# Performance work log

Hardware: AMD Instinct MI355X
Metric: run time of the kernel (lower is better)

## Reference

```python
import jax, jax.numpy as jnp
import numpy as np

N, E = 20000, 320000
D, DW, DS, NCLS = 512, 300, 16, 13


def setup_inputs() -> dict:
    key = jax.random.key(0)
    ks = jax.random.split(key, 24)
    g = lambda k, s, sc=0.02: (jax.random.normal(k, s, dtype=jnp.float32) * sc)
    inp = {
        'n_f': jax.random.normal(ks[0], (N, D), dtype=jnp.float32),
        'word2vec': jax.random.normal(ks[1], (N, DW), dtype=jnp.float32),
        's_f': jax.random.normal(ks[2], (E, DS), dtype=jnp.float32),
        'src': jax.random.randint(ks[3], (E,), 0, N, dtype=jnp.int32),
        'dst': jax.random.randint(ks[4], (E,), 0, N, dtype=jnp.int32),
        # edge MLPs: G_E_L_S=[2*D+DS, D], G_E_L_S2=[2*DW, D]
        'W_e': g(ks[5], (2 * D + DS, D)), 'b_e': jnp.zeros((D,), jnp.float32),
        'W_el': g(ks[6], (2 * DW, D)), 'b_el': jnp.zeros((D,), jnp.float32),
        # attention MLPs: G_A_L_S=[D,1], G_A_L_S2=[D,1]
        'W_a': g(ks[7], (D, 1)), 'b_a': jnp.zeros((1,), jnp.float32),
        'W_al': g(ks[8], (D, 1)), 'b_al': jnp.zeros((1,), jnp.float32),
        # node MLPs: G_N_L_S=[2*D, D], G_N_L_S2=[2*DW, DW]
        'W_n': g(ks[9], (2 * D, D)), 'b_n': jnp.zeros((D,), jnp.float32),
        'W_nl': g(ks[10], (2 * DW, DW)), 'b_nl': jnp.zeros((DW,), jnp.float32),
        # edge readout: G_ER_L_S=[2*D+2*DW+DS, D, 13], acts ['ReLU','Identity']
        'W_r1': g(ks[11], (2 * D + 2 * DW + DS, D)), 'b_r1': jnp.zeros((D,), jnp.float32),
        'W_r2': g(ks[12], (D, NCLS)), 'b_r2': jnp.zeros((NCLS,), jnp.float32),
    }
    return inp


def _segment_softmax(logits, seg, num_segments):
    m = jax.ops.segment_max(logits, seg, num_segments=num_segments)
    m = jnp.where(jnp.isfinite(m), m, 0.0)
    e = jnp.exp(logits - m[seg])
    s = jax.ops.segment_sum(e, seg, num_segments=num_segments)
    return e / (s[seg] + 1e-9)


def _forward(n_f, word2vec, s_f, W_e, b_e, W_el, b_el, W_a, b_a, W_al, b_al,
             W_n, b_n, W_nl, b_nl, W_r1, b_r1, W_r2, b_r2, src, dst):
    n = n_f.shape[0]
    relu = jax.nn.relu
    # H_H_EdgeApplyModule: e_f = ReLU(MLP([src n_f, s_f, dst n_f]))
    feat = jnp.concatenate([n_f[src], s_f, n_f[dst]], axis=1)            # [E, 2D+DS]
    e_f = relu(feat @ W_e + b_e)                                         # [E, D]
    feat_lang = jnp.concatenate([word2vec[src], word2vec[dst]], axis=1)  # [E, 2DW]
    e_f_lang = relu(feat_lang @ W_el + b_el)                             # [E, D]
    # E_AttentionModule1: LeakyReLU(0.2) attention logits per edge
    a = jax.nn.leaky_relu(e_f @ W_a + b_a, 0.2)[:, 0]
    a_l = jax.nn.leaky_relu(e_f_lang @ W_al + b_al, 0.2)[:, 0]
    # edge-softmax over incoming edges of each destination node
    alpha = _segment_softmax(a, dst, n)
    alpha_l = _segment_softmax(a_l, dst, n)
    # attention-weighted aggregation (scatter-add per dst node)
    z = jax.ops.segment_sum(alpha[:, None] * e_f, dst, num_segments=n)            # [N, D]
    z_l = jax.ops.segment_sum(alpha_l[:, None] * word2vec[src], dst, num_segments=n)  # [N, DW]
    # H_NodeApplyModule: node update with ReLU MLPs
    n_new = relu(jnp.concatenate([n_f, z], axis=1) @ W_n + b_n)          # [N, D]
    w_new = relu(jnp.concatenate([word2vec, z_l], axis=1) @ W_nl + b_nl) # [N, DW]
    # edge readout (G_ER): [src n_f, src w2v, s_f, dst w2v, dst n_f] -> ReLU -> Identity
    r = jnp.concatenate([n_new[src], w_new[src], s_f, w_new[dst], n_new[dst]], axis=1)
    h = relu(r @ W_r1 + b_r1)
    return h @ W_r2 + b_r2                                               # [E, 13]


def reference(n_f, word2vec, s_f, src, dst, W_e, b_e, W_el, b_el, W_a, b_a,
              W_al, b_al, W_n, b_n, W_nl, b_nl, W_r1, b_r1, W_r2, b_r2):
    return _forward(n_f, word2vec, s_f, W_e, b_e, W_el, b_el, W_a, b_a, W_al, b_al,
                    W_n, b_n, W_nl, b_nl, W_r1, b_r1, W_r2, b_r2, src, dst)
```

## Files before the change

kernel.cpp:

```cpp
#include <hip/hip_runtime.h>

typedef unsigned short u16;
typedef unsigned int u32;
typedef __bf16 bf16x8 __attribute__((ext_vector_type(8)));
typedef float f32x4 __attribute__((ext_vector_type(4)));

#define ND 512
#define DWR 300
#define DWP 320
#define NCLS 13

__device__ __forceinline__ float bf2f(u16 u) { return __uint_as_float(((u32)u) << 16); }
__device__ __forceinline__ u16 f2bf(float f) {
    u32 u = __float_as_uint(f);
    u32 r = (u + 0x7FFFu + ((u >> 16) & 1u)) >> 16;
    return (u16)r;
}
__device__ __forceinline__ void ub8(float4 r, float* v) {
    union { float4 f; u16 u[8]; } U; U.f = r;
#pragma unroll
    for (int k = 0; k < 8; ++k) v[k] = bf2f(U.u[k]);
}
__device__ __forceinline__ void ld8f(const u16* p, float* v) { ub8(*(const float4*)p, v); }
__device__ __forceinline__ void ld16(const float* p, float* s) {
    const float4* sp = (const float4*)p;
    float4 s0 = sp[0], s1 = sp[1], s2 = sp[2], s3 = sp[3];
    s[0]=s0.x; s[1]=s0.y; s[2]=s0.z; s[3]=s0.w; s[4]=s1.x; s[5]=s1.y; s[6]=s1.z; s[7]=s1.w;
    s[8]=s2.x; s[9]=s2.y; s[10]=s2.z; s[11]=s2.w; s[12]=s3.x; s[13]=s3.y; s[14]=s3.z; s[15]=s3.w;
}

struct GSeg { const u16* base; const int* idx; int stride; int width; };
struct GSegs { GSeg s[5]; };
struct TSeg { int src_begin; int wreal; int wpad; };
struct TSegs { TSeg t[5]; };

template<int RELU>
__global__ __launch_bounds__(256) void gemm_k(
    int M, int Nout, GSegs segs,
    const u16* __restrict__ BT, int ldb,
    const float* __restrict__ bias, int bias_n,
    u16* __restrict__ outb, int ldo)
{
    __shared__ __align__(16) u16 As[128 * 40];
    __shared__ __align__(16) u16 Bs[128 * 40];
    const int tid = threadIdx.x;

    const int gx = gridDim.x, gy = gridDim.y;
    const int g0 = blockIdx.x + gx * blockIdx.y;
    int xt, yt;
    {
        const int fullg = gx >> 3;
        const int gsz = 8 * gy;
        if (g0 < fullg * gsz) {
            const int grp = g0 / gsz, w = g0 % gsz;
            xt = grp * 8 + (w & 7); yt = w >> 3;
        } else {
            const int remx = gx - fullg * 8;
            const int t = g0 - fullg * gsz;
            xt = fullg * 8 + t % remx; yt = t / remx;
        }
    }
    const int m0 = xt * 128, n0 = yt * 128;

    const int row = tid >> 1, half = tid & 1;
    int mrow = m0 + row; if (mrow >= M) mrow = M - 1;
    const int lane = tid & 63, wid = tid >> 6;
    const int wr = (wid >> 1) * 64, wc = (wid & 1) * 64;
    const int lr = lane & 15, lg = lane >> 4;

    f32x4 acc[4][4];
    for (int fm = 0; fm < 4; fm++)
        for (int fn = 0; fn < 4; fn++)
            acc[fm][fn] = f32x4{0.f, 0.f, 0.f, 0.f};

    const u16* brow = BT + (size_t)(n0 + row) * ldb + half * 16;

    auto do_step = [&](const u16* ga_, const u16* gb_) {
        float4 a0 = *(const float4*)ga_;
        float4 a1 = *(const float4*)(ga_ + 8);
        float4 b0 = *(const float4*)gb_;
        float4 b1 = *(const float4*)(gb_ + 8);
        __syncthreads();
        *(float4*)&As[row * 40 + half * 16]     = a0;
        *(float4*)&As[row * 40 + half * 16 + 8] = a1;
        *(float4*)&Bs[row * 40 + half * 16]     = b0;
        *(float4*)&Bs[row * 40 + half * 16 + 8] = b1;
        __syncthreads();
        bf16x8 af[4], bfv[4];
#pragma unroll
        for (int f = 0; f < 4; f++) {
            af[f]  = *(const bf16x8*)&As[(wr + f * 16 + lr) * 40 + lg * 8];
            bfv[f] = *(const bf16x8*)&Bs[(wc + f * 16 + lr) * 40 + lg * 8];
        }
#pragma unroll
        for (int fm = 0; fm < 4; fm++)
#pragma unroll
            for (int fn = 0; fn < 4; fn++)
                acc[fm][fn] = __builtin_amdgcn_mfma_f32_16x16x32_bf16(af[fm], bfv[fn], acc[fm][fn], 0, 0, 0);
    };

    int k0 = 0;
#pragma unroll
    for (int sI = 0; sI < 5; sI++) {
        const GSeg S = segs.s[sI];
        if (S.width > 0) {
            const int ridx = S.idx ? S.idx[mrow] : mrow;
            const u16* abase = S.base + (size_t)ridx * S.stride + half * 16;
            for (int kk = 0; kk < S.width; kk += 32) {
                do_step(abase + kk, brow + k0 + kk);
            }
            k0 += S.width;
        }
    }

#pragma unroll
    for (int fm = 0; fm < 4; fm++) {
#pragma unroll
        for (int i = 0; i < 4; i++) {
            const int grow = m0 + wr + fm * 16 + lg * 4 + i;
            const bool rok = grow < M;
#pragma unroll
            for (int fn = 0; fn < 4; fn++) {
                const int col = n0 + wc + fn * 16 + lr;
                float v = acc[fm][fn][i];
                v += (col < bias_n) ? bias[col] : 0.f;
                if (RELU) v = fmaxf(v, 0.f);
                if (rok && col < Nout) outb[(size_t)grow * ldo + col] = f2bf(v);
            }
        }
    }
}

__global__ __launch_bounds__(256) void pass1_k(
    const u16* __restrict__ Q, const u16* __restrict__ Lq,
    const float* __restrict__ s_f, const float* __restrict__ wmid,
    const int* __restrict__ psrc, const int* __restrict__ pdst, const int* __restrict__ perm,
    const float* __restrict__ W_a, const float* __restrict__ W_al,
    const float* __restrict__ b_e, const float* __restrict__ b_el,
    const float* __restrict__ b_a, const float* __restrict__ b_al,
    float* __restrict__ aA, float* __restrict__ aL, int E)
{
    __shared__ __align__(16) u16 wmids[16 * 520];
    __shared__ __align__(16) u16 As_v[128 * 40];
    __shared__ __align__(16) u16 As_l[128 * 40];
    __shared__ float sfs[16 * 128];
    __shared__ float bes[512], bels[512];
    __shared__ __align__(16) u16 was[512], wals[512];

    const int tid = threadIdx.x;
    const int e0 = blockIdx.x * 128;

    for (int i = tid; i < 16 * 512; i += 256)
        wmids[(i >> 9) * 520 + (i & 511)] = f2bf(wmid[i]);
    for (int i = tid; i < 512; i += 256) {
        bes[i] = b_e[i]; bels[i] = b_el[i];
        was[i] = f2bf(W_a[i]); wals[i] = f2bf(W_al[i]);
    }

    const int row = tid >> 1, half = tid & 1;
    const int er = e0 + row;
    const int erc = (er < E) ? er : E - 1;
    {
        const int pe = perm[erc];
        const int jh = half * 8;
        const float4* sp = (const float4*)(s_f + (size_t)pe * 16 + jh);
        float4 a = sp[0], b = sp[1];
        sfs[(jh + 0) * 128 + row] = a.x; sfs[(jh + 1) * 128 + row] = a.y;
        sfs[(jh + 2) * 128 + row] = a.z; sfs[(jh + 3) * 128 + row] = a.w;
        sfs[(jh + 4) * 128 + row] = b.x; sfs[(jh + 5) * 128 + row] = b.y;
        sfs[(jh + 6) * 128 + row] = b.z; sfs[(jh + 7) * 128 + row] = b.w;
    }

    const int ps = psrc[erc], pd = pdst[erc];
    const u16* q1b = Q + (size_t)ps * 1024;
    const u16* q2b = Q + (size_t)pd * 1024 + 512;
    const u16* l1b = Lq + (size_t)ps * 1024;
    const u16* l2b = Lq + (size_t)pd * 1024 + 512;

    const int lane = tid & 63, wid = tid >> 6;
    const int lr = lane & 15, lg = lane >> 4;
    f32x4 accv[2], accl[2];
    accv[0] = accv[1] = accl[0] = accl[1] = f32x4{0.f, 0.f, 0.f, 0.f};

    union { bf16x8 v; float4 f; } BZ; BZ.f = float4{0.f, 0.f, 0.f, 0.f};

    __syncthreads();

    for (int ch = 0; ch < 16; ++ch) {
        const int k0 = ch * 32 + half * 16;
        float4 rq1a = *(const float4*)(q1b + k0);
        float4 rq1b = *(const float4*)(q1b + k0 + 8);
        float4 rq2a = *(const float4*)(q2b + k0);
        float4 rq2b = *(const float4*)(q2b + k0 + 8);
        float4 rl1a = *(const float4*)(l1b + k0);
        float4 rl1b = *(const float4*)(l1b + k0 + 8);
        float4 rl2a = *(const float4*)(l2b + k0);
        float4 rl2b = *(const float4*)(l2b + k0 + 8);

        float uv[16], ul[16], t1[8], t2[8];
        ub8(rq1a, t1); ub8(rq2a, t2);
#pragma unroll
        for (int k = 0; k < 8; ++k) uv[k] = t1[k] + t2[k] + bes[k0 + k];
        ub8(rq1b, t1); ub8(rq2b, t2);
#pragma unroll
        for (int k = 0; k < 8; ++k) uv[8 + k] = t1[k] + t2[k] + bes[k0 + 8 + k];
        ub8(rl1a, t1); ub8(rl2a, t2);
#pragma unroll
        for (int k = 0; k < 8; ++k) ul[k] = t1[k] + t2[k] + bels[k0 + k];
        ub8(rl1b, t1); ub8(rl2b, t2);
#pragma unroll
        for (int k = 0; k < 8; ++k) ul[8 + k] = t1[k] + t2[k] + bels[k0 + 8 + k];

#pragma unroll
        for (int j = 0; j < 16; ++j) {
            const float sv = sfs[j * 128 + row];
            union { float4 f; u16 u[8]; } W1, W2;
            W1.f = *(const float4*)&wmids[j * 520 + k0];
            W2.f = *(const float4*)&wmids[j * 520 + k0 + 8];
#pragma unroll
            for (int k = 0; k < 8; ++k) {
                uv[k]     = fmaf(sv, bf2f(W1.u[k]), uv[k]);
                uv[8 + k] = fmaf(sv, bf2f(W2.u[k]), uv[8 + k]);
            }
        }
        union { float4 f; u16 u[8]; } Va, Vb, La, Lb;
#pragma unroll
        for (int k = 0; k < 8; ++k) {
            Va.u[k] = f2bf(fmaxf(uv[k], 0.f));
            Vb.u[k] = f2bf(fmaxf(uv[8 + k], 0.f));
            La.u[k] = f2bf(fmaxf(ul[k], 0.f));
            Lb.u[k] = f2bf(fmaxf(ul[8 + k], 0.f));
        }
        __syncthreads();
        *(float4*)&As_v[row * 40 + half * 16]     = Va.f;
        *(float4*)&As_v[row * 40 + half * 16 + 8] = Vb.f;
        *(float4*)&As_l[row * 40 + half * 16]     = La.f;
        *(float4*)&As_l[row * 40 + half * 16 + 8] = Lb.f;
        __syncthreads();

        bf16x8 bv = BZ.v, bl = BZ.v;
        if (lr == 0) {
            bv = *(const bf16x8*)&was[ch * 32 + lg * 8];
            bl = *(const bf16x8*)&wals[ch * 32 + lg * 8];
        }
#pragma unroll
        for (int m = 0; m < 2; ++m) {
            bf16x8 afv = *(const bf16x8*)&As_v[(wid * 32 + m * 16 + lr) * 40 + lg * 8];
            bf16x8 afl = *(const bf16x8*)&As_l[(wid * 32 + m * 16 + lr) * 40 + lg * 8];
            accv[m] = __builtin_amdgcn_mfma_f32_16x16x32_bf16(afv, bv, accv[m], 0, 0, 0);
            accl[m] = __builtin_amdgcn_mfma_f32_16x16x32_bf16(afl, bl, accl[m], 0, 0, 0);
        }
    }

    if (lr == 0) {
        const float ba = b_a[0], bal = b_al[0];
#pragma unroll
        for (int m = 0; m < 2; ++m) {
#pragma unroll
            for (int i = 0; i < 4; ++i) {
                const int e = e0 + wid * 32 + m * 16 + lg * 4 + i;
                if (e < E) {
                    float x = accv[m][i] + ba;
                    aA[e] = x > 0.f ? x : 0.2f * x;
                    float y = accl[m][i] + bal;
                    aL[e] = y > 0.f ? y : 0.2f * y;
                }
            }
        }
    }
}

__global__ __launch_bounds__(256) void softmax_k(
    float* __restrict__ a, float* __restrict__ al,
    const int* __restrict__ offs, int N, int E)
{
    const int node = blockIdx.x * 4 + (threadIdx.x >> 6);
    if (node >= N) return;
    const int lane = threadIdx.x & 63;
    const int e0 = offs[node];
    const int e1 = (node + 1 < N) ? offs[node + 1] : E;
    if (e0 >= e1) return;
    float m = -3.4e38f, ml = -3.4e38f;
    for (int e = e0 + lane; e < e1; e += 64) { m = fmaxf(m, a[e]); ml = fmaxf(ml, al[e]); }
#pragma unroll
    for (int off = 32; off >= 1; off >>= 1) {
        m  = fmaxf(m,  __shfl_xor(m,  off, 64));
        ml = fmaxf(ml, __shfl_xor(ml, off, 64));
    }
    float s = 0.f, sl = 0.f;
    for (int e = e0 + lane; e < e1; e += 64) {
        float v = expf(a[e] - m);   a[e] = v;  s += v;
        float w = expf(al[e] - ml); al[e] = w; sl += w;
    }
#pragma unroll
    for (int off = 32; off >= 1; off >>= 1) {
        s  += __shfl_xor(s,  off, 64);
        sl += __shfl_xor(sl, off, 64);
    }
    const float rs = 1.f / (s + 1e-9f), rsl = 1.f / (sl + 1e-9f);
    for (int e = e0 + lane; e < e1; e += 64) { a[e] *= rs; al[e] *= rsl; }
}

__global__ __launch_bounds__(256) void passz_k(
    const u16* __restrict__ Q, const u16* __restrict__ wv_bf,
    const float* __restrict__ s_f, const float* __restrict__ wmid,
    const int* __restrict__ psrc, const int* __restrict__ perm, const int* __restrict__ offs,
    const float* __restrict__ alpha, const float* __restrict__ alphal,
    const float* __restrict__ b_e,
    u16* __restrict__ z_bf, u16* __restrict__ zl_bf, int N, int E)
{
    __shared__ __align__(16) u16 wmids[16 * 512];
    const int tid = threadIdx.x;
    for (int i = tid; i < 16 * 512; i += 256) wmids[i] = f2bf(wmid[i]);
    __syncthreads();
    const int node = blockIdx.x * 4 + (tid >> 6);
    if (node >= N) return;
    const int lane = tid & 63;
    const int col0 = lane * 8;
    const int colw = (lane < 40) ? col0 : 0;
    const int e0 = offs[node];
    const int e1 = (node + 1 < N) ? offs[node + 1] : E;

    float q2b[8], accz[8], accl[8], t[8];
    ld8f(Q + (size_t)node * 1024 + 512 + col0, q2b);
#pragma unroll
    for (int k = 0; k < 8; ++k) { q2b[k] += b_e[col0 + k]; accz[k] = 0.f; accl[k] = 0.f; }

    if (e0 < e1) {
        int ps0 = psrc[e0], pe0 = perm[e0];
        float4 rq0 = *(const float4*)(Q + (size_t)ps0 * 1024 + col0);
        float4 rw0 = *(const float4*)(wv_bf + (size_t)ps0 * DWP + colw);
        int ps1 = ps0, pe1 = pe0;
        if (e0 + 1 < e1) { ps1 = psrc[e0 + 1]; pe1 = perm[e0 + 1]; }

        for (int e = e0; e < e1; ++e) {
            float4 rq1 = rq0, rw1 = rw0;
            if (e + 1 < e1) {
                rq1 = *(const float4*)(Q + (size_t)ps1 * 1024 + col0);
                rw1 = *(const float4*)(wv_bf + (size_t)ps1 * DWP + colw);
            }
            int ps2 = ps1, pe2 = pe1;
            if (e + 2 < e1) { ps2 = psrc[e + 2]; pe2 = perm[e + 2]; }

            const float alA = alpha[e], alL = alphal[e];
            float sf[16];
            ld16(s_f + (size_t)pe0 * 16, sf);
            float v[8];
            ub8(rq0, t);
#pragma unroll
            for (int k = 0; k < 8; ++k) v[k] = t[k] + q2b[k];
#pragma unroll
            for (int j = 0; j < 16; ++j) {
                union { float4 f; u16 u[8]; } W;
                W.f = *(const float4*)&wmids[j * 512 + col0];
#pragma unroll
                for (int k = 0; k < 8; ++k) v[k] = fmaf(sf[j], bf2f(W.u[k]), v[k]);
            }
#pragma unroll
            for (int k = 0; k < 8; ++k) accz[k] = fmaf(alA, fmaxf(v[k], 0.f), accz[k]);
            ub8(rw0, t);
#pragma unroll
            for (int k = 0; k < 8; ++k) accl[k] = fmaf(alL, t[k], accl[k]);

            rq0 = rq1; rw0 = rw1; ps0 = ps1; pe0 = pe1; ps1 = ps2; pe1 = pe2;
        }
    }
    union { float4 f; u16 u[8]; } O;
#pragma unroll
    for (int k = 0; k < 8; ++k) O.u[k] = f2bf(accz[k]);
    *(float4*)(z_bf + (size_t)node * 512 + col0) = O.f;
    if (lane < 40) {
#pragma unroll
        for (int k = 0; k < 8; ++k) O.u[k] = f2bf(accl[k]);
        *(float4*)(zl_bf + (size_t)node * DWP + col0) = O.f;
    }
}

__global__ __launch_bounds__(256) void pass3_k(
    const u16* __restrict__ P, const float* __restrict__ s_f, const float* __restrict__ wmid2,
    const int* __restrict__ psrc, const int* __restrict__ pdst, const int* __restrict__ perm,
    const float* __restrict__ b_r1, const float* __restrict__ w2, const float* __restrict__ b_r2,
    float* __restrict__ out, int E)
{
    __shared__ __align__(16) u16 As[128 * 40];
    __shared__ __align__(16) u16 wmid2s[16 * 520];
    __shared__ __align__(16) u16 w2Ts[16 * 520];
    __shared__ float sfs[16 * 128];
    __shared__ float br1s[512];

    const int tid = threadIdx.x;
    const int e0 = blockIdx.x * 128;

    for (int i = tid; i < 16 * 512; i += 256)
        wmid2s[(i >> 9) * 520 + (i & 511)] = f2bf(wmid2[i]);
    for (int i = tid; i < 16 * 512; i += 256) {
        const int c = i >> 9, k = i & 511;
        w2Ts[c * 520 + k] = f2bf((c < NCLS) ? w2[k * NCLS + c] : 0.f);
    }
    for (int i = tid; i < 512; i += 256) br1s[i] = b_r1[i];

    const int row = tid >> 1, half = tid & 1;
    const int er = e0 + row;
    const int erc = (er < E) ? er : E - 1;
    {
        const int pe = perm[erc];
        const int jh = half * 8;
        const float4* sp = (const float4*)(s_f + (size_t)pe * 16 + jh);
        float4 a = sp[0], b = sp[1];
        sfs[(jh + 0) * 128 + row] = a.x; sfs[(jh + 1) * 128 + row] = a.y;
        sfs[(jh + 2) * 128 + row] = a.z; sfs[(jh + 3) * 128 + row] = a.w;
        sfs[(jh + 4) * 128 + row] = b.x; sfs[(jh + 5) * 128 + row] = b.y;
        sfs[(jh + 6) * 128 + row] = b.z; sfs[(jh + 7) * 128 + row] = b.w;
    }

    const int ps = psrc[erc], pd = pdst[erc];
    const u16* p1base = P + (size_t)ps * 1024;
    const u16* p2base = P + (size_t)pd * 1024 + 512;

    const int lane = tid & 63, wid = tid >> 6;
    const int lr = lane & 15, lg = lane >> 4;
    f32x4 acc0 = f32x4{0.f, 0.f, 0.f, 0.f};
    f32x4 acc1 = f32x4{0.f, 0.f, 0.f, 0.f};

    __syncthreads();

    for (int ch = 0; ch < 16; ++ch) {
        const int k0 = ch * 32 + half * 16;
        float4 r1a = *(const float4*)(p1base + k0);
        float4 r1b = *(const float4*)(p1base + k0 + 8);
        float4 r2a = *(const float4*)(p2base + k0);
        float4 r2b = *(const float4*)(p2base + k0 + 8);
        float u[16], t1[8], t2[8];
        ub8(r1a, t1); ub8(r2a, t2);
#pragma unroll
        for (int k = 0; k < 8; ++k) u[k] = t1[k] + t2[k] + br1s[k0 + k];
        ub8(r1b, t1); ub8(r2b, t2);
#pragma unroll
        for (int k = 0; k < 8; ++k) u[8 + k] = t1[k] + t2[k] + br1s[k0 + 8 + k];
#pragma unroll
        for (int j = 0; j < 16; ++j) {
            const float sv = sfs[j * 128 + row];
            union { float4 f; u16 u[8]; } W1, W2;
            W1.f = *(const float4*)&wmid2s[j * 520 + k0];
            W2.f = *(const float4*)&wmid2s[j * 520 + k0 + 8];
#pragma unroll
            for (int k = 0; k < 8; ++k) {
                u[k]     = fmaf(sv, bf2f(W1.u[k]), u[k]);
                u[8 + k] = fmaf(sv, bf2f(W2.u[k]), u[8 + k]);
            }
        }
        union { float4 f; u16 u[8]; } Oa, Ob;
#pragma unroll
        for (int k = 0; k < 8; ++k) {
            Oa.u[k] = f2bf(fmaxf(u[k], 0.f));
            Ob.u[k] = f2bf(fmaxf(u[8 + k], 0.f));
        }
        __syncthreads();
        *(float4*)&As[row * 40 + half * 16]     = Oa.f;
        *(float4*)&As[row * 40 + half * 16 + 8] = Ob.f;
        __syncthreads();
        bf16x8 af0 = *(const bf16x8*)&As[(wid * 32 +      lr) * 40 + lg * 8];
        bf16x8 af1 = *(const bf16x8*)&As[(wid * 32 + 16 + lr) * 40 + lg * 8];
        bf16x8 bfv = *(const bf16x8*)&w2Ts[lr * 520 + ch * 32 + lg * 8];
        acc0 = __builtin_amdgcn_mfma_f32_16x16x32_bf16(af0, bfv, acc0, 0, 0, 0);
        acc1 = __builtin_amdgcn_mfma_f32_16x16x32_bf16(af1, bfv, acc1, 0, 0, 0);
    }

    if (lr < NCLS) {
        const float bc = b_r2[lr];
#pragma unroll
        for (int m = 0; m < 2; ++m) {
            const f32x4 a = m ? acc1 : acc0;
            const int rbase = e0 + wid * 32 + m * 16 + lg * 4;
#pragma unroll
            for (int i = 0; i < 4; ++i) {
                const int ei = rbase + i;
                if (ei < E) out[(size_t)perm[ei] * NCLS + lr] = a[i] + bc;
            }
        }
    }
}

__global__ __launch_bounds__(256) void cvt_bf(const float* __restrict__ src, u16* __restrict__ dst,
                                              int R, int Cs, int Cd)
{
    int id = blockIdx.x * 256 + threadIdx.x;
    if (id >= R * Cd) return;
    int r = id / Cd, c = id % Cd;
    float v = (c < Cs) ? src[(size_t)r * Cs + c] : 0.f;
    dst[id] = f2bf(v);
}

__global__ __launch_bounds__(256) void wtrans(const float* __restrict__ W, int Nw, int Nreal,
                                              int NrowsOut, int ldk, TSegs ts, int nseg,
                                              u16* __restrict__ WT)
{
    int id = blockIdx.x * 256 + threadIdx.x;
    if (id >= NrowsOut * ldk) return;
    int n = id / ldk, kp = id % ldk;
    float v = 0.f;
    if (n < Nreal) {
        int off = 0;
#pragma unroll
        for (int s = 0; s < 5; s++) {
            if (s < nseg) {
                int kl = kp - off;
                if (kl >= 0 && kl < ts.t[s].wpad) {
                    if (kl < ts.t[s].wreal) v = W[(size_t)(ts.t[s].src_begin + kl) * Nw + n];
                }
                off += ts.t[s].wpad;
            }
        }
    }
    WT[id] = f2bf(v);
}

__global__ __launch_bounds__(256) void hist_k(const int* __restrict__ dst, int* __restrict__ deg, int E)
{
    int id = blockIdx.x * 256 + threadIdx.x;
    if (id < E) atomicAdd(&deg[dst[id]], 1);
}

__global__ __launch_bounds__(1024) void scan_k(const int* __restrict__ deg,
                                               int* __restrict__ offs, int* __restrict__ cursor, int N)
{
    __shared__ int ps[1024];
    const int t = threadIdx.x;
    const int per = (N + 1023) >> 10;
    int s = 0;
    for (int j = 0; j < per; j++) { int idx = t * per + j; if (idx < N) s += deg[idx]; }
    ps[t] = s; __syncthreads();
    for (int o = 1; o < 1024; o <<= 1) {
        int v = (t >= o) ? ps[t - o] : 0; __syncthreads();
        ps[t] += v; __syncthreads();
    }
    int run = ps[t] - s;
    for (int j = 0; j < per; j++) {
        int idx = t * per + j;
        if (idx < N) { offs[idx] = run; cursor[idx] = run; run += deg[idx]; }
    }
}

__global__ __launch_bounds__(256) void scat_perm_k(const int* __restrict__ src, const int* __restrict__ dst,
                                                   int* __restrict__ cursor, int* __restrict__ perm,
                                                   int* __restrict__ psrc, int* __restrict__ pdst, int E)
{
    int id = blockIdx.x * 256 + threadIdx.x;
    if (id >= E) return;
    int d = dst[id];
    int pos = atomicAdd(&cursor[d], 1);
    perm[pos] = id; psrc[pos] = src[id]; pdst[pos] = d;
}

__global__ __launch_bounds__(256) void diag_fill(float* out, int n, float v)
{
    int id = blockIdx.x * 256 + threadIdx.x;
    if (id < n) out[id] = v;
}

extern "C" void kernel_launch(void* const* d_in, const int* in_sizes, int n_in,
                              void* d_out, int out_size, void* d_ws, size_t ws_size,
                              hipStream_t stream)
{
    const float* n_f  = (const float*)d_in[0];
    const float* w2v  = (const float*)d_in[1];
    const float* s_f  = (const float*)d_in[2];
    const int*   src  = (const int*)d_in[3];
    const int*   dst  = (const int*)d_in[4];
    const float* W_e  = (const float*)d_in[5];
    const float* b_e  = (const float*)d_in[6];
    const float* W_el = (const float*)d_in[7];
    const float* b_el = (const float*)d_in[8];
    const float* W_a  = (const float*)d_in[9];
    const float* b_a  = (const float*)d_in[10];
    const float* W_al = (const float*)d_in[11];
    const float* b_al = (const float*)d_in[12];
    const float* W_n  = (const float*)d_in[13];
    const float* b_n  = (const float*)d_in[14];
    const float* W_nl = (const float*)d_in[15];
    const float* b_nl = (const float*)d_in[16];
    const float* W_r1 = (const float*)d_in[17];
    const float* b_r1 = (const float*)d_in[18];
    const float* W_r2 = (const float*)d_in[19];
    const float* b_r2 = (const float*)d_in[20];

    const int N = in_sizes[0] / ND;
    const int E = in_sizes[3];
    float* out = (float*)d_out;

    auto g1 = [](long long n) { return dim3((unsigned)((n + 255) / 256)); };

    char* base = (char*)d_ws;
    size_t off = 0;
    auto alloc = [&](size_t bytes) -> void* {
        void* r = base + off;
        off += (bytes + 255) & ~(size_t)255;
        return r;
    };
    u16* nf_bf = (u16*)alloc((size_t)N * ND * 2);
    u16* wv_bf = (u16*)alloc((size_t)N * DWP * 2);
    u16* Q     = (u16*)alloc((size_t)N * 1024 * 2);
    u16* Lq    = (u16*)alloc((size_t)N * 1024 * 2);
    u16* Pt    = (u16*)alloc((size_t)N * 1024 * 2);
    u16* z_bf  = (u16*)alloc((size_t)N * ND * 2);
    u16* zl_bf = (u16*)alloc((size_t)N * DWP * 2);
    u16* nn_bf = (u16*)alloc((size_t)N * ND * 2);
    u16* wn_bf = (u16*)alloc((size_t)N * DWP * 2);
    u16* QT    = (u16*)alloc((size_t)1024 * 512 * 2);
    u16* LT    = (u16*)alloc((size_t)1024 * 320 * 2);
    u16* WnT   = (u16*)alloc((size_t)512 * 1024 * 2);
    u16* WnlT  = (u16*)alloc((size_t)384 * 640 * 2);
    u16* PrT   = (u16*)alloc((size_t)1024 * 832 * 2);
    float* aAs = (float*)alloc((size_t)E * 4);
    float* aLs = (float*)alloc((size_t)E * 4);
    int* deg    = (int*)alloc((size_t)N * 4);
    int* offs   = (int*)alloc((size_t)N * 4);
    int* cursor = (int*)alloc((size_t)N * 4);
    int* perm   = (int*)alloc((size_t)E * 4);
    int* psrc   = (int*)alloc((size_t)E * 4);
    int* pdst   = (int*)alloc((size_t)E * 4);

    if (off > ws_size) {
        diag_fill<<<g1(out_size), 256, 0, stream>>>(out, out_size, 2.0e6f);
        return;
    }

    hipMemsetAsync(deg, 0, (size_t)N * 4, stream);

    hist_k<<<g1(E), 256, 0, stream>>>(dst, deg, E);
    scan_k<<<dim3(1), 1024, 0, stream>>>(deg, offs, cursor, N);
    scat_perm_k<<<g1(E), 256, 0, stream>>>(src, dst, cursor, perm, psrc, pdst, E);

    cvt_bf<<<g1((long long)N * ND), 256, 0, stream>>>(n_f, nf_bf, N, ND, ND);
    cvt_bf<<<g1((long long)N * DWP), 256, 0, stream>>>(w2v, wv_bf, N, DWR, DWP);

    { TSegs t{}; t.t[0] = {0,512,512};
      wtrans<<<g1(512 * 512), 256, 0, stream>>>(W_e, 512, 512, 512, 512, t, 1, QT); }
    { TSegs t{}; t.t[0] = {528,512,512};
      wtrans<<<g1(512 * 512), 256, 0, stream>>>(W_e, 512, 512, 512, 512, t, 1, QT + 512 * 512); }
    { TSegs t{}; t.t[0] = {0,300,320};
      wtrans<<<g1(512 * 320), 256, 0, stream>>>(W_el, 512, 512, 512, 320, t, 1, LT); }
    { TSegs t{}; t.t[0] = {300,300,320};
      wtrans<<<g1(512 * 320), 256, 0, stream>>>(W_el, 512, 512, 512, 320, t, 1, LT + 512 * 320); }
    { TSegs t{}; t.t[0] = {0,512,512}; t.t[1] = {512,512,512};
      wtrans<<<g1(512 * 1024), 256, 0, stream>>>(W_n, 512, 512, 512, 1024, t, 2, WnT); }
    { TSegs t{}; t.t[0] = {0,300,320}; t.t[1] = {300,300,320};
      wtrans<<<g1(384 * 640), 256, 0, stream>>>(W_nl, 300, 300, 384, 640, t, 2, WnlT); }
    { TSegs t{}; t.t[0] = {0,512,512}; t.t[1] = {512,300,320};
      wtrans<<<g1(512 * 832), 256, 0, stream>>>(W_r1, 512, 512, 512, 832, t, 2, PrT); }
    { TSegs t{}; t.t[0] = {1128,512,512}; t.t[1] = {828,300,320};
      wtrans<<<g1(512 * 832), 256, 0, stream>>>(W_r1, 512, 512, 512, 832, t, 2, PrT + 512 * 832); }

    const int gmx = (N + 127) / 128;
    const dim3 gnode((N + 3) / 4);

    { GSegs s{}; s.s[0] = {nf_bf, nullptr, ND, 512};
      gemm_k<0><<<dim3(gmx, 8), 256, 0, stream>>>(N, 1024, s, QT, 512, nullptr, 0, Q, 1024); }
    { GSegs s{}; s.s[0] = {wv_bf, nullptr, DWP, 320};
      gemm_k<0><<<dim3(gmx, 8), 256, 0, stream>>>(N, 1024, s, LT, 320, nullptr, 0, Lq, 1024); }

    pass1_k<<<dim3((E + 127) / 128), 256, 0, stream>>>(Q, Lq, s_f, W_e + 512 * 512,
                                                       psrc, pdst, perm, W_a, W_al,
                                                       b_e, b_el, b_a, b_al, aAs, aLs, E);
    softmax_k<<<gnode, 256, 0, stream>>>(aAs, aLs, offs, N, E);

    passz_k<<<gnode, 256, 0, stream>>>(Q, wv_bf, s_f, W_e + 512 * 512, psrc, perm, offs,
                                       aAs, aLs, b_e, z_bf, zl_bf, N, E);

    { GSegs s{}; s.s[0] = {nf_bf, nullptr, ND, 512}; s.s[1] = {z_bf, nullptr, ND, 512};
      gemm_k<1><<<dim3(gmx, 4), 256, 0, stream>>>(N, 512, s, WnT, 1024, b_n, 512, nn_bf, 512); }
    { GSegs s{}; s.s[0] = {wv_bf, nullptr, DWP, 320}; s.s[1] = {zl_bf, nullptr, DWP, 320};
      gemm_k<1><<<dim3(gmx, 3), 256, 0, stream>>>(N, 320, s, WnlT, 640, b_nl, 300, wn_bf, DWP); }

    { GSegs s{}; s.s[0] = {nn_bf, nullptr, ND, 512}; s.s[1] = {wn_bf, nullptr, DWP, 320};
      gemm_k<0><<<dim3(gmx, 8), 256, 0, stream>>>(N, 1024, s, PrT, 832, nullptr, 0, Pt, 1024); }

    pass3_k<<<dim3((E + 127) / 128), 256, 0, stream>>>(Pt, s_f, W_r1 + 812 * 512,
                                                       psrc, pdst, perm, b_r1, W_r2, b_r2, out, E);

    hipError_t e = hipGetLastError();
    if (e != hipSuccess) {
        diag_fill<<<g1(out_size), 256, 0, stream>>>(out, out_size, 1.0e6f + (float)(int)e);
    }
}
```

Measured before the change: 1.009 ms.

## Compute s_f projection with MFMA instead of scalar FMA loops in edge passes

In both edge kernels, the per-edge 16-wide s_f times weight-slice product was computed with scalar FMAs reading bf16 weights from LDS. Now s_f is staged as zero-padded bf16 tiles and multiplied by a transposed weight tile with 16x16x32 bf16 MFMAs each chunk; the result goes through an LDS buffer (sfw) that each thread reads back and adds. This moves the work onto the matrix cores and cuts VALU instructions, at the cost of extra LDS traffic, larger shared-memory use, half-wasted MFMA K dimension, and s_f now rounded to bf16. Barrier placement is reshuffled to protect the new buffer.

```diff
diff --git a/kernel.cpp b/kernel.cpp
--- a/kernel.cpp
+++ b/kernel.cpp
@@ -140,18 +140,21 @@
     const float* __restrict__ b_a, const float* __restrict__ b_al,
     float* __restrict__ aA, float* __restrict__ aL, int E)
 {
-    __shared__ __align__(16) u16 wmids[16 * 520];
+    __shared__ __align__(16) u16 sfs_bf[128 * 40];
+    __shared__ __align__(16) u16 wmidT[512 * 16];
     __shared__ __align__(16) u16 As_v[128 * 40];
     __shared__ __align__(16) u16 As_l[128 * 40];
-    __shared__ float sfs[16 * 128];
+    __shared__ __align__(16) float sfw[128 * 36];
     __shared__ float bes[512], bels[512];
     __shared__ __align__(16) u16 was[512], wals[512];
 
     const int tid = threadIdx.x;
     const int e0 = blockIdx.x * 128;
 
-    for (int i = tid; i < 16 * 512; i += 256)
-        wmids[(i >> 9) * 520 + (i & 511)] = f2bf(wmid[i]);
+    for (int i = tid; i < 512 * 16; i += 256) {
+        const int col = i >> 4, k = i & 15;
+        wmidT[i] = f2bf(wmid[k * 512 + col]);
+    }
     for (int i = tid; i < 512; i += 256) {
         bes[i] = b_e[i]; bels[i] = b_el[i];
         was[i] = f2bf(W_a[i]); wals[i] = f2bf(W_al[i]);
@@ -162,13 +165,14 @@
     const int erc = (er < E) ? er : E - 1;
     {
         const int pe = perm[erc];
-        const int jh = half * 8;
-        const float4* sp = (const float4*)(s_f + (size_t)pe * 16 + jh);
+        const float4* sp = (const float4*)(s_f + (size_t)pe * 16 + half * 8);
         float4 a = sp[0], b = sp[1];
-        sfs[(jh + 0) * 128 + row] = a.x; sfs[(jh + 1) * 128 + row] = a.y;
-        sfs[(jh + 2) * 128 + row] = a.z; sfs[(jh + 3) * 128 + row] = a.w;
-        sfs[(jh + 4) * 128 + row] = b.x; sfs[(jh + 5) * 128 + row] = b.y;
-        sfs[(jh + 6) * 128 + row] = b.z; sfs[(jh + 7) * 128 + row] = b.w;
+        union { float4 f; u16 u[8]; } S;
+        S.u[0]=f2bf(a.x); S.u[1]=f2bf(a.y); S.u[2]=f2bf(a.z); S.u[3]=f2bf(a.w);
+        S.u[4]=f2bf(b.x); S.u[5]=f2bf(b.y); S.u[6]=f2bf(b.z); S.u[7]=f2bf(b.w);
+        *(float4*)&sfs_bf[row * 40 + half * 8] = S.f;
+        S.f = float4{0.f, 0.f, 0.f, 0.f};
+        *(float4*)&sfs_bf[row * 40 + 16 + half * 8] = S.f;
     }
 
     const int ps = psrc[erc], pd = pdst[erc];
@@ -181,13 +185,27 @@
     const int lr = lane & 15, lg = lane >> 4;
     f32x4 accv[2], accl[2];
     accv[0] = accv[1] = accl[0] = accl[1] = f32x4{0.f, 0.f, 0.f, 0.f};
-
     union { bf16x8 v; float4 f; } BZ; BZ.f = float4{0.f, 0.f, 0.f, 0.f};
 
     __syncthreads();
 
     for (int ch = 0; ch < 16; ++ch) {
         const int k0 = ch * 32 + half * 16;
+#pragma unroll
+        for (int rt = 0; rt < 2; ++rt) {
+            bf16x8 af = *(const bf16x8*)&sfs_bf[((wid * 2 + rt) * 16 + lr) * 40 + lg * 8];
+#pragma unroll
+            for (int ct = 0; ct < 2; ++ct) {
+                const int f = ch * 32 + ct * 16 + lr;
+                bf16x8 bf_ = *(const bf16x8*)&wmidT[f * 16 + (lg & 1) * 8];
+                f32x4 c = __builtin_amdgcn_mfma_f32_16x16x32_bf16(af, bf_, f32x4{0.f,0.f,0.f,0.f}, 0, 0, 0);
+#pragma unroll
+                for (int i = 0; i < 4; ++i)
+                    sfw[((wid * 2 + rt) * 16 + lg * 4 + i) * 36 + ct * 16 + lr] = c[i];
+            }
+        }
+        __syncthreads();
+
         float4 rq1a = *(const float4*)(q1b + k0);
         float4 rq1b = *(const float4*)(q1b + k0 + 8);
         float4 rq2a = *(const float4*)(q2b + k0);
@@ -196,14 +214,19 @@
         float4 rl1b = *(const float4*)(l1b + k0 + 8);
         float4 rl2a = *(const float4*)(l2b + k0);
         float4 rl2b = *(const float4*)(l2b + k0 + 8);
+        float sw[16];
+        *(float4*)&sw[0]  = *(const float4*)&sfw[row * 36 + half * 16 + 0];
+        *(float4*)&sw[4]  = *(const float4*)&sfw[row * 36 + half * 16 + 4];
+        *(float4*)&sw[8]  = *(const float4*)&sfw[row * 36 + half * 16 + 8];
+        *(float4*)&sw[12] = *(const float4*)&sfw[row * 36 + half * 16 + 12];
 
         float uv[16], ul[16], t1[8], t2[8];
         ub8(rq1a, t1); ub8(rq2a, t2);
 #pragma unroll
-        for (int k = 0; k < 8; ++k) uv[k] = t1[k] + t2[k] + bes[k0 + k];
+        for (int k = 0; k < 8; ++k) uv[k] = t1[k] + t2[k] + bes[k0 + k] + sw[k];
         ub8(rq1b, t1); ub8(rq2b, t2);
 #pragma unroll
-        for (int k = 0; k < 8; ++k) uv[8 + k] = t1[k] + t2[k] + bes[k0 + 8 + k];
+        for (int k = 0; k < 8; ++k) uv[8 + k] = t1[k] + t2[k] + bes[k0 + 8 + k] + sw[8 + k];
         ub8(rl1a, t1); ub8(rl2a, t2);
 #pragma unroll
         for (int k = 0; k < 8; ++k) ul[k] = t1[k] + t2[k] + bels[k0 + k];
@@ -211,18 +234,6 @@
 #pragma unroll
         for (int k = 0; k < 8; ++k) ul[8 + k] = t1[k] + t2[k] + bels[k0 + 8 + k];
 
-#pragma unroll
-        for (int j = 0; j < 16; ++j) {
-            const float sv = sfs[j * 128 + row];
-            union { float4 f; u16 u[8]; } W1, W2;
-            W1.f = *(const float4*)&wmids[j * 520 + k0];
-            W2.f = *(const float4*)&wmids[j * 520 + k0 + 8];
-#pragma unroll
-            for (int k = 0; k < 8; ++k) {
-                uv[k]     = fmaf(sv, bf2f(W1.u[k]), uv[k]);
-                uv[8 + k] = fmaf(sv, bf2f(W2.u[k]), uv[8 + k]);
-            }
-        }
         union { float4 f; u16 u[8]; } Va, Vb, La, Lb;
 #pragma unroll
         for (int k = 0; k < 8; ++k) {
@@ -231,7 +242,6 @@
             La.u[k] = f2bf(fmaxf(ul[k], 0.f));
             Lb.u[k] = f2bf(fmaxf(ul[8 + k], 0.f));
         }
-        __syncthreads();
         *(float4*)&As_v[row * 40 + half * 16]     = Va.f;
         *(float4*)&As_v[row * 40 + half * 16 + 8] = Vb.f;
         *(float4*)&As_l[row * 40 + half * 16]     = La.f;
@@ -383,16 +393,19 @@
     float* __restrict__ out, int E)
 {
     __shared__ __align__(16) u16 As[128 * 40];
-    __shared__ __align__(16) u16 wmid2s[16 * 520];
+    __shared__ __align__(16) u16 sfs_bf[128 * 40];
+    __shared__ __align__(16) u16 wmidT[512 * 16];
     __shared__ __align__(16) u16 w2Ts[16 * 520];
-    __shared__ float sfs[16 * 128];
+    __shared__ __align__(16) float sfw[128 * 36];
     __shared__ float br1s[512];
 
     const int tid = threadIdx.x;
     const int e0 = blockIdx.x * 128;
 
-    for (int i = tid; i < 16 * 512; i += 256)
-        wmid2s[(i >> 9) * 520 + (i & 511)] = f2bf(wmid2[i]);
+    for (int i = tid; i < 512 * 16; i += 256) {
+        const int col = i >> 4, k = i & 15;
+        wmidT[i] = f2bf(wmid2[k * 512 + col]);
+    }
     for (int i = tid; i < 16 * 512; i += 256) {
         const int c = i >> 9, k = i & 511;
         w2Ts[c * 520 + k] = f2bf((c < NCLS) ? w2[k * NCLS + c] : 0.f);
@@ -404,13 +417,14 @@
     const int erc = (er < E) ? er : E - 1;
     {
         const int pe = perm[erc];
-        const int jh = half * 8;
-        const float4* sp = (const float4*)(s_f + (size_t)pe * 16 + jh);
+        const float4* sp = (const float4*)(s_f + (size_t)pe * 16 + half * 8);
         float4 a = sp[0], b = sp[1];
-        sfs[(jh + 0) * 128 + row] = a.x; sfs[(jh + 1) * 128 + row] = a.y;
-        sfs[(jh + 2) * 128 + row] = a.z; sfs[(jh + 3) * 128 + row] = a.w;
-        sfs[(jh + 4) * 128 + row] = b.x; sfs[(jh + 5) * 128 + row] = b.y;
-        sfs[(jh + 6) * 128 + row] = b.z; sfs[(jh + 7) * 128 + row] = b.w;
+        union { float4 f; u16 u[8]; } S;
+        S.u[0]=f2bf(a.x); S.u[1]=f2bf(a.y); S.u[2]=f2bf(a.z); S.u[3]=f2bf(a.w);
+        S.u[4]=f2bf(b.x); S.u[5]=f2bf(b.y); S.u[6]=f2bf(b.z); S.u[7]=f2bf(b.w);
+        *(float4*)&sfs_bf[row * 40 + half * 8] = S.f;
+        S.f = float4{0.f, 0.f, 0.f, 0.f};
+        *(float4*)&sfs_bf[row * 40 + 16 + half * 8] = S.f;
     }
 
     const int ps = psrc[erc], pd = pdst[erc];
@@ -426,39 +440,49 @@
 
     for (int ch = 0; ch < 16; ++ch) {
         const int k0 = ch * 32 + half * 16;
+#pragma unroll
+        for (int rt = 0; rt < 2; ++rt) {
+            bf16x8 af = *(const bf16x8*)&sfs_bf[((wid * 2 + rt) * 16 + lr) * 40 + lg * 8];
+#pragma unroll
+            for (int ct = 0; ct < 2; ++ct) {
+                const int f = ch * 32 + ct * 16 + lr;
+                bf16x8 bf_ = *(const bf16x8*)&wmidT[f * 16 + (lg & 1) * 8];
+                f32x4 c = __builtin_amdgcn_mfma_f32_16x16x32_bf16(af, bf_, f32x4{0.f,0.f,0.f,0.f}, 0, 0, 0);
+#pragma unroll
+                for (int i = 0; i < 4; ++i)
+                    sfw[((wid * 2 + rt) * 16 + lg * 4 + i) * 36 + ct * 16 + lr] = c[i];
+            }
+        }
+        __syncthreads();
+
         float4 r1a = *(const float4*)(p1base + k0);
         float4 r1b = *(const float4*)(p1base + k0 + 8);
         float4 r2a = *(const float4*)(p2base + k0);
         float4 r2b = *(const float4*)(p2base + k0 + 8);
+        float sw[16];
+        *(float4*)&sw[0]  = *(const float4*)&sfw[row * 36 + half * 16 + 0];
+        *(float4*)&sw[4]  = *(const float4*)&sfw[row * 36 + half * 16 + 4];
+        *(float4*)&sw[8]  = *(const float4*)&sfw[row * 36 + half * 16 + 8];
+        *(float4*)&sw[12] = *(const float4*)&sfw[row * 36 + half * 16 + 12];
+
         float u[16], t1[8], t2[8];
         ub8(r1a, t1); ub8(r2a, t2);
 #pragma unroll
-        for (int k = 0; k < 8; ++k) u[k] = t1[k] + t2[k] + br1s[k0 + k];
+        for (int k = 0; k < 8; ++k) u[k] = t1[k] + t2[k] + br1s[k0 + k] + sw[k];
         ub8(r1b, t1); ub8(r2b, t2);
 #pragma unroll
-        for (int k = 0; k < 8; ++k) u[8 + k] = t1[k] + t2[k] + br1s[k0 + 8 + k];
-#pragma unroll
-        for (int j = 0; j < 16; ++j) {
-            const float sv = sfs[j * 128 + row];
-            union { float4 f; u16 u[8]; } W1, W2;
-            W1.f = *(const float4*)&wmid2s[j * 520 + k0];
-            W2.f = *(const float4*)&wmid2s[j * 520 + k0 + 8];
-#pragma unroll
-            for (int k = 0; k < 8; ++k) {
-                u[k]     = fmaf(sv, bf2f(W1.u[k]), u[k]);
-                u[8 + k] = fmaf(sv, bf2f(W2.u[k]), u[8 + k]);
-            }
-        }
+        for (int k = 0; k < 8; ++k) u[8 + k] = t1[k] + t2[k] + br1s[k0 + 8 + k] + sw[8 + k];
+
         union { float4 f; u16 u[8]; } Oa, Ob;
 #pragma unroll
         for (int k = 0; k < 8; ++k) {
             Oa.u[k] = f2bf(fmaxf(u[k], 0.f));
             Ob.u[k] = f2bf(fmaxf(u[8 + k], 0.f));
         }
-        __syncthreads();
         *(float4*)&As[row * 40 + half * 16]     = Oa.f;
         *(float4*)&As[row * 40 + half * 16 + 8] = Ob.f;
         __syncthreads();
+
         bf16x8 af0 = *(const bf16x8*)&As[(wid * 32 +      lr) * 40 + lg * 8];
         bf16x8 af1 = *(const bf16x8*)&As[(wid * 32 + 16 + lr) * 40 + lg * 8];
         bf16x8 bfv = *(const bf16x8*)&w2Ts[lr * 520 + ch * 32 + lg * 8];
```

Result: faster. 939.7 us (-6.9%).
